# Kernel tuning notes

Hardware: AMD Instinct MI355X
Metric: run time of the kernel (lower is better)

Reference implementation:

```python
import jax, jax.numpy as jnp
import numpy as np

EPS = 1e-6
K = 3
R_MIN, R_MAX = 0.5, 2.0


def setup_inputs() -> dict:
    key = jax.random.key(0)
    k0, k1, k2, k3 = jax.random.split(key, 4)
    N, C, D, H, W = 2, 32, 48, 48, 48
    T = 1 + K + 3 + 1  # num_tokens = 6
    x = jax.random.normal(k0, (N, C, D, H, W), jnp.float32)
    w_field = jax.random.normal(k1, (4 * K, C), jnp.float32) * 0.05
    b_field = jnp.zeros((4 * K,), jnp.float32)
    gates = jax.random.normal(k2, (T,), jnp.float32)
    w_mix = jax.random.normal(k3, (C, T * C), jnp.float32) * 0.02
    b_mix = jnp.zeros((C,), jnp.float32)
    return {"x": x, "w_field": w_field, "b_field": b_field, "gates": gates, "w_mix": w_mix, "b_mix": b_mix}


def _reflect(coord, size):
    # torch 'reflection' padding, align_corners=False: reflect over [-0.5, size-0.5]
    c = jnp.abs(coord + 0.5)
    m = jnp.mod(c, 2.0 * size)
    return jnp.minimum(m, 2.0 * size - m) - 0.5


def _trilinear_sample(vol, gx, gy, gz):
    # vol: (N, D, H, W, C) channels-last; gx/gy/gz: (N, K, D, H, W) normalized coords in [-1, 1]
    N, D, H, W, C = vol.shape

    def unnorm(g, size):
        return _reflect(((g + 1.0) * size - 1.0) * 0.5, float(size))

    ix, iy, iz = unnorm(gx, W), unnorm(gy, H), unnorm(gz, D)
    x0 = jnp.floor(ix); y0 = jnp.floor(iy); z0 = jnp.floor(iz)
    fx = (ix - x0)[..., None]; fy = (iy - y0)[..., None]; fz = (iz - z0)[..., None]
    x0i = jnp.clip(x0.astype(jnp.int32), 0, W - 1); x1i = jnp.clip(x0i + 1, 0, W - 1)
    y0i = jnp.clip(y0.astype(jnp.int32), 0, H - 1); y1i = jnp.clip(y0i + 1, 0, H - 1)
    z0i = jnp.clip(z0.astype(jnp.int32), 0, D - 1); z1i = jnp.clip(z0i + 1, 0, D - 1)
    n = jnp.arange(N).reshape(N, 1, 1, 1, 1)

    def g(zi, yi, xi):
        return vol[n, zi, yi, xi]  # (N, K, D, H, W, C)

    c00 = g(z0i, y0i, x0i) * (1.0 - fx) + g(z0i, y0i, x1i) * fx
    c01 = g(z0i, y1i, x0i) * (1.0 - fx) + g(z0i, y1i, x1i) * fx
    c10 = g(z1i, y0i, x0i) * (1.0 - fx) + g(z1i, y0i, x1i) * fx
    c11 = g(z1i, y1i, x0i) * (1.0 - fx) + g(z1i, y1i, x1i) * fx
    c0 = c00 * (1.0 - fy) + c01 * fy
    c1 = c10 * (1.0 - fy) + c11 * fy
    return c0 * (1.0 - fz) + c1 * fz


def reference(x, w_field, b_field, gates, w_mix, b_mix):
    N, C, D, H, W = x.shape
    # field head: 1x1x1 conv C -> 4K, split into K unit directions U and radii r
    f = jnp.einsum('ncdhw,oc->nodhw', x, w_field) + b_field[None, :, None, None, None]
    f = f.reshape(N, K, 4, D, H, W)
    v = f[:, :, :3]
    U = v / jnp.sqrt(jnp.sum(v * v, axis=2, keepdims=True) + EPS)  # (N,K,3,D,H,W)
    r_s = R_MIN + (R_MAX - R_MIN) * jax.nn.sigmoid(f[:, :, 3])     # (N,K,D,H,W)
    # base grid, align_corners=False normalized coordinates
    gz0 = ((jnp.arange(D, dtype=x.dtype) + 0.5) * 2.0 / D - 1.0)[:, None, None]
    gy0 = ((jnp.arange(H, dtype=x.dtype) + 0.5) * 2.0 / H - 1.0)[None, :, None]
    gx0 = ((jnp.arange(W, dtype=x.dtype) + 0.5) * 2.0 / W - 1.0)[None, None, :]
    ux, uy, uz = U[:, :, 0], U[:, :, 1], U[:, :, 2]
    dx = 2.0 * r_s * ux / (W + EPS)
    dy = 2.0 * r_s * uy / (H + EPS)
    dz = 2.0 * r_s * uz / (D + EPS)
    vol = jnp.transpose(x, (0, 2, 3, 4, 1))  # (N,D,H,W,C)
    xp = _trilinear_sample(vol, gx0 + dx, gy0 + dy, gz0 + dz)  # (N,K,D,H,W,C)
    xm = _trilinear_sample(vol, gx0 - dx, gy0 - dy, gz0 - dz)
    xp = jnp.transpose(xp, (0, 1, 5, 2, 3, 4))  # (N,K,C,D,H,W)
    xm = jnp.transpose(xm, (0, 1, 5, 2, 3, 4))
    a = 0.5 * (xp + xm)
    o = 0.5 * (xp - xm)
    inv_r = 1.0 / (jax.lax.stop_gradient(r_s) + EPS)  # r detached in original
    d1 = o * inv_r[:, :, None]                        # (N,K,C,D,H,W)
    G = jnp.einsum('nkadhw,nkcdhw->nacdhw', U, d1)     # (N,3,C,D,H,W)
    d2 = (xp + xm - 2.0 * x[:, None]) * (inv_r * inv_r)[:, :, None]
    L = d2.mean(axis=1)                                # (N,C,D,H,W)
    tokens = jnp.concatenate([x[:, None], a, G, L[:, None]], axis=1)  # (N,T,C,D,H,W)
    T = tokens.shape[1]
    gated = tokens * jax.nn.sigmoid(gates)[None, :, None, None, None, None]
    delta = jnp.einsum('nmdhw,om->nodhw', gated.reshape(N, T * C, D, H, W), w_mix)
    delta = delta + b_mix[None, :, None, None, None]
    return x + delta
```

## Files before the change

### kernel.cpp

```cpp
#include <hip/hip_runtime.h>
#include <math.h>

#define NB   2
#define CH   32
#define DHW  (48*48*48)
#define TT   8
#define EPSF 1e-6f

#define TILE_N   1521
#define TILE_WSTR 1522
#define GROUPS   8

#define TOK_OFF  0
#define TOK_STR  64
#define TILE_OFF 16384
#define SMEM_SZ  40736

#define WS_BT_F 0
#define WS_WF   4096
#define WS_BF   4480
#define WS_BM   4492

typedef __attribute__((ext_vector_type(8))) short short8;
typedef __attribute__((ext_vector_type(8))) _Float16 half8;
typedef __attribute__((ext_vector_type(4))) float floatx4;
typedef __attribute__((ext_vector_type(2))) _Float16 h2;

struct __align__(8) q4 { h2 lo, hi; };

__device__ __forceinline__ h2 pkrtz(float a, float b) {
    return __builtin_bit_cast(h2, __builtin_amdgcn_cvt_pkrtz(a, b));
}
__device__ __forceinline__ unsigned pkrtz_u(float a, float b) {
    return __builtin_bit_cast(unsigned, __builtin_amdgcn_cvt_pkrtz(a, b));
}

__global__ __launch_bounds__(256) void prep_kernel(
        const float* __restrict__ w_field,
        const float* __restrict__ b_field,
        const float* __restrict__ gates,
        const float* __restrict__ w_mix,
        const float* __restrict__ b_mix,
        float* __restrict__ ws) {
    int i = blockIdx.x * 256 + threadIdx.x;
    {
        int o = i >> 8, k = i & 255, c = k >> 3, t = k & 7;
        float sg = 1.0f / (1.0f + expf(-gates[t]));
        _Float16 hv = (_Float16)(sg * w_mix[o * 256 + t * 32 + c]);
        ((unsigned short*)(ws + WS_BT_F))[o * 256 + k] = __builtin_bit_cast(unsigned short, hv);
    }
    if (i < 384) { int c = i / 12, o = i - c * 12; ws[WS_WF + i] = w_field[o * 32 + c]; }
    if (i < 12)  ws[WS_BF + i] = b_field[i];
    if (i < 32)  ws[WS_BM + i] = b_mix[i];
}

__global__ __launch_bounds__(256) void geo_main(
        const float* __restrict__ x,
        const float* __restrict__ ws,
        float* __restrict__ out) {
    __shared__ __align__(16) char smem[SMEM_SZ];
    char* tokb  = smem + TOK_OFF;
    q4*   tileq = (q4*)(smem + TILE_OFF);
    float* cbuf = (float*)smem;

    const int tid = threadIdx.x;
    const int lin = (blockIdx.x & 7) * 108 + (blockIdx.x >> 3);
    const int bx = lin % 6, by = (lin / 6) % 6, bz = (lin / 36) % 12, n = lin / 432;
    const int lx = tid & 7, ly = (tid >> 3) & 7, lz = tid >> 6;
    const int w = bx * 8 + lx, h = by * 8 + ly, d = bz * 4 + lz;
    const int xlo = bx * 8 - 2, ylo = by * 8 - 2, zlo = bz * 4 - 2;
    const int lane = tid & 63, w64 = tid & 192;

    const float* xn = x + (size_t)n * CH * DHW;

    int goff[6];
#pragma unroll
    for (int i = 0; i < 6; ++i) {
        int e  = tid + i * 256;
        int ee = (e < TILE_N) ? e : 0;
        int tz = ee / 169; int r0 = ee - tz * 169;
        int ty = r0 / 13;  int tx = r0 - ty * 13;
        int zg = min(max(zlo + tz, 0), 47);
        int yg = min(max(ylo + ty, 0), 47);
        int xg = min(max(xlo + tx, 0), 47);
        goff[i] = (zg * 48 + yg) * 48 + xg;
    }

    const int pos = (d * 48 + h) * 48 + w;
    float f[12];
#pragma unroll
    for (int o = 0; o < 12; ++o) f[o] = ws[WS_BF + o];
    for (int c = 0; c < CH; ++c) {
        float xv = xn[c * DHW + pos];
        const float* wf = ws + WS_WF + c * 12;
#pragma unroll
        for (int o = 0; o < 12; ++o) f[o] = fmaf(wf[o], xv, f[o]);
    }

    h2 fx2[6], fy2[6], fz2[6];
    int a00[6], a01[6], a10[6], a11[6];
    float uxk[3], uyk[3], uzk[3], irk[3], ir2k[3];
    const float cscale = 48.0f / (48.0f + EPSF);
#pragma unroll
    for (int k = 0; k < 3; ++k) {
        float vx = f[4*k], vy = f[4*k+1], vz = f[4*k+2], s = f[4*k+3];
        float inv = 1.0f / sqrtf(vx*vx + vy*vy + vz*vz + EPSF);
        float ux = vx * inv, uy = vy * inv, uz = vz * inv;
        float r  = 0.5f + 1.5f / (1.0f + expf(-s));
        uxk[k] = ux; uyk[k] = uy; uzk[k] = uz;
        float ir = 1.0f / (r + EPSF); irk[k] = ir; ir2k[k] = ir * ir;
#pragma unroll
        for (int sgn = 0; sgn < 2; ++sgn) {
            int   si = 2 * k + sgn;
            float sf = sgn ? -1.0f : 1.0f;
            float txr = (float)w + sf * r * ux * cscale;
            float tyr = (float)h + sf * r * uy * cscale;
            float tzr = (float)d + sf * r * uz * cscale;
            float cx = fabsf(txr + 0.5f); float ix = fminf(cx, 96.0f - cx) - 0.5f;
            float cy = fabsf(tyr + 0.5f); float iy = fminf(cy, 96.0f - cy) - 0.5f;
            float cz = fabsf(tzr + 0.5f); float iz = fminf(cz, 96.0f - cz) - 0.5f;
            float x0f = floorf(ix), y0f = floorf(iy), z0f = floorf(iz);
            float fx = ix - x0f, fy = iy - y0f, fz = iz - z0f;
            int x0 = min(max((int)x0f, 0), 47); int x1 = min(x0 + 1, 47);
            int y0 = min(max((int)y0f, 0), 47); int y1 = min(y0 + 1, 47);
            int z0 = min(max((int)z0f, 0), 47); int z1 = min(z0 + 1, 47);
            float fxe = (x1 == x0) ? 0.0f : fx;
            _Float16 hx = (_Float16)fxe, hy = (_Float16)fy, hz = (_Float16)fz;
            fx2[si] = (h2){hx, hx}; fy2[si] = (h2){hy, hy}; fz2[si] = (h2){hz, hz};
            int lz0 = z0 - zlo, lz1 = z1 - zlo;
            int ly0 = y0 - ylo, ly1 = y1 - ylo;
            int lx0 = x0 - xlo;
            a00[si] = (lz0 * 13 + ly0) * 13 + lx0;
            a01[si] = (lz0 * 13 + ly1) * 13 + lx0;
            a10[si] = (lz1 * 13 + ly0) * 13 + lx0;
            a11[si] = (lz1 * 13 + ly1) * 13 + lx0;
        }
    }

    if (tid == 0) {
        q4 z; z.lo = (h2){0, 0}; z.hi = (h2){0, 0};
        tileq[TILE_N] = z; tileq[TILE_WSTR + TILE_N] = z;
    }
    {
        float ld[24];
#pragma unroll
        for (int cg = 0; cg < 4; ++cg) {
            const float* xc = xn + cg * DHW;
#pragma unroll
            for (int i = 0; i < 6; ++i) ld[cg * 6 + i] = xc[goff[i]];
        }
#pragma unroll
        for (int i = 0; i < 6; ++i) {
            int e = tid + i * 256;
            if (e < TILE_N) {
                q4 v; v.lo = pkrtz(ld[i], ld[6 + i]); v.hi = pkrtz(ld[12 + i], ld[18 + i]);
                tileq[e] = v;
            }
        }
    }
    __syncthreads();

    floatx4 acc[4][2];
#pragma unroll
    for (int mt = 0; mt < 4; ++mt)
#pragma unroll
        for (int nt = 0; nt < 2; ++nt) acc[mt][nt] = (floatx4){0.f, 0.f, 0.f, 0.f};

    const int self = ((lz + 2) * 13 + (ly + 2)) * 13 + (lx + 2);
    const unsigned short* bt = (const unsigned short*)(ws + WS_BT_F);
    const int tokq = (tid >> 3) & 3;
    const int qm = lane >> 4, nlo = lane & 15;

    short8 bc0 = *(const short8*)(bt + (nlo * 256 + qm * 8));
    short8 bc1 = *(const short8*)(bt + ((nlo + 16) * 256 + qm * 8));

    for (int g = 0; g < GROUPS; ++g) {
        const int rb = (g & 1);
        const int wb = rb ^ 1;
        float nld[24];
        short8 bn0 = bc0, bn1 = bc1;
        if (g < GROUPS - 1) {
            const float* xg = xn + (g + 1) * 4 * DHW;
#pragma unroll
            for (int cg = 0; cg < 4; ++cg) {
                const float* xc = xg + cg * DHW;
#pragma unroll
                for (int i = 0; i < 6; ++i) nld[cg * 6 + i] = xc[goff[i]];
            }
            bn0 = *(const short8*)(bt + (nlo * 256 + (g + 1) * 32 + qm * 8));
            bn1 = *(const short8*)(bt + ((nlo + 16) * 256 + (g + 1) * 32 + qm * 8));
        }
        const q4* tb = tileq + rb * TILE_WSTR;
        q4 s2 = tb[self];
        q4 vv[6];
#pragma unroll
        for (int si = 0; si < 6; ++si) {
            int b00 = a00[si], b01 = a01[si], b10 = a10[si], b11 = a11[si];
            q4 v000 = tb[b00], v001 = tb[b00 + 1];
            q4 v010 = tb[b01], v011 = tb[b01 + 1];
            q4 v100 = tb[b10], v101 = tb[b10 + 1];
            q4 v110 = tb[b11], v111 = tb[b11 + 1];
            h2 fx = fx2[si], fy = fy2[si], fz = fz2[si];
            h2 c00l = v000.lo + fx * (v001.lo - v000.lo);
            h2 c00h = v000.hi + fx * (v001.hi - v000.hi);
            h2 c01l = v010.lo + fx * (v011.lo - v010.lo);
            h2 c01h = v010.hi + fx * (v011.hi - v010.hi);
            h2 c10l = v100.lo + fx * (v101.lo - v100.lo);
            h2 c10h = v100.hi + fx * (v101.hi - v100.hi);
            h2 c11l = v110.lo + fx * (v111.lo - v110.lo);
            h2 c11h = v110.hi + fx * (v111.hi - v110.hi);
            h2 c0l = c00l + fy * (c01l - c00l);
            h2 c0h = c00h + fy * (c01h - c00h);
            h2 c1l = c10l + fy * (c11l - c10l);
            h2 c1h = c10h + fy * (c11h - c10h);
            vv[si].lo = c0l + fz * (c1l - c0l);
            vv[si].hi = c0h + fz * (c1h - c0h);
        }
#pragma unroll
        for (int sub = 0; sub < 4; ++sub) {
            float xv = (sub == 0) ? (float)s2.lo.x : (sub == 1) ? (float)s2.lo.y
                     : (sub == 2) ? (float)s2.hi.x : (float)s2.hi.y;
            float val[6];
#pragma unroll
            for (int si = 0; si < 6; ++si)
                val[si] = (sub == 0) ? (float)vv[si].lo.x : (sub == 1) ? (float)vv[si].lo.y
                        : (sub == 2) ? (float)vv[si].hi.x : (float)vv[si].hi.y;
            float t1, t2, t3, gx, gy, gz, l;
            {
                float sp, sm, d1;
                sp = val[0]; sm = val[1]; t1 = 0.5f * (sp + sm);
                d1 = 0.5f * (sp - sm) * irk[0];
                gx = uxk[0] * d1; gy = uyk[0] * d1; gz = uzk[0] * d1;
                l  = (sp + sm - 2.0f * xv) * ir2k[0];
                sp = val[2]; sm = val[3]; t2 = 0.5f * (sp + sm);
                d1 = 0.5f * (sp - sm) * irk[1];
                gx = fmaf(uxk[1], d1, gx); gy = fmaf(uyk[1], d1, gy); gz = fmaf(uzk[1], d1, gz);
                l  = fmaf(sp + sm - 2.0f * xv, ir2k[1], l);
                sp = val[4]; sm = val[5]; t3 = 0.5f * (sp + sm);
                d1 = 0.5f * (sp - sm) * irk[2];
                gx = fmaf(uxk[2], d1, gx); gy = fmaf(uyk[2], d1, gy); gz = fmaf(uzk[2], d1, gz);
                l  = fmaf(sp + sm - 2.0f * xv, ir2k[2], l);
            }
            uint4 tw;
            tw.x = pkrtz_u(xv, t1);
            tw.y = pkrtz_u(t2, t3);
            tw.z = pkrtz_u(gx, gy);
            tw.w = pkrtz_u(gz, l * (1.0f / 3.0f));
            int qe = sub ^ tokq;
            *(uint4*)(tokb + tid * TOK_STR + qe * 16) = tw;
        }
        {
            half8 hb0 = __builtin_bit_cast(half8, bc0);
            half8 hb1 = __builtin_bit_cast(half8, bc1);
#pragma unroll
            for (int mt = 0; mt < 4; ++mt) {
                int row = w64 + mt * 16 + nlo;
                int qe  = qm ^ ((row >> 3) & 3);
                half8 a = __builtin_bit_cast(half8,
                          *(const short8*)(tokb + row * TOK_STR + qe * 16));
                acc[mt][0] = __builtin_amdgcn_mfma_f32_16x16x32_f16(a, hb0, acc[mt][0], 0, 0, 0);
                acc[mt][1] = __builtin_amdgcn_mfma_f32_16x16x32_f16(a, hb1, acc[mt][1], 0, 0, 0);
            }
        }
        bc0 = bn0; bc1 = bn1;

        if (g < GROUPS - 1) {
#pragma unroll
            for (int i = 0; i < 6; ++i) {
                int e = tid + i * 256;
                if (e < TILE_N) {
                    q4 v; v.lo = pkrtz(nld[i], nld[6 + i]); v.hi = pkrtz(nld[12 + i], nld[18 + i]);
                    tileq[wb * TILE_WSTR + e] = v;
                }
            }
        }
        __syncthreads();
    }

    {
#pragma unroll
        for (int mt = 0; mt < 4; ++mt)
#pragma unroll
            for (int nt = 0; nt < 2; ++nt)
#pragma unroll
                for (int r = 0; r < 4; ++r) {
                    int v = w64 + mt * 16 + qm * 4 + r;
                    int col = nt * 16 + nlo;
                    cbuf[v * 36 + (col ^ (v & 31))] = acc[mt][nt][r];
                }
    }
    __syncthreads();

    const float* dr = cbuf + tid * 36;
    float* on = out + (size_t)n * CH * DHW;
#pragma unroll
    for (int o = 0; o < 32; ++o)
        __builtin_nontemporal_store(
            xn[o * DHW + pos] + dr[o ^ (tid & 31)] + ws[WS_BM + o],
            on + o * DHW + pos);
}

extern "C" void kernel_launch(void* const* d_in, const int* in_sizes, int n_in,
                              void* d_out, int out_size, void* d_ws, size_t ws_size,
                              hipStream_t stream) {
    const float *x = (const float*)d_in[0], *w_field = (const float*)d_in[1],
                *b_field = (const float*)d_in[2], *gates = (const float*)d_in[3],
                *w_mix = (const float*)d_in[4], *b_mix = (const float*)d_in[5];
    for (int i = 0; i < n_in; ++i) {
        switch (in_sizes[i]) {
            case NB * CH * DHW: x       = (const float*)d_in[i]; break;
            case 12 * CH:       w_field = (const float*)d_in[i]; break;
            case 12:            b_field = (const float*)d_in[i]; break;
            case TT:            gates   = (const float*)d_in[i]; break;
            case CH * TT * CH:  w_mix   = (const float*)d_in[i]; break;
            case CH:            b_mix   = (const float*)d_in[i]; break;
            default: break;
        }
    }
    float* ws = (float*)d_ws;
    prep_kernel<<<32, 256, 0, stream>>>(w_field, b_field, gates, w_mix, b_mix, ws);
    geo_main<<<864, 256, 0, stream>>>(x, ws, (float*)d_out);
}
```

Baseline: 157.0 us.

## Compute token features in packed fp16 and precompute bilinear yz weights

Result: slower. 237.3 us (+51.2%).

```diff
diff --git a/kernel.cpp b/kernel.cpp
--- a/kernel.cpp
+++ b/kernel.cpp
@@ -31,8 +31,11 @@
 __device__ __forceinline__ h2 pkrtz(float a, float b) {
     return __builtin_bit_cast(h2, __builtin_amdgcn_cvt_pkrtz(a, b));
 }
-__device__ __forceinline__ unsigned pkrtz_u(float a, float b) {
-    return __builtin_bit_cast(unsigned, __builtin_amdgcn_cvt_pkrtz(a, b));
+__device__ __forceinline__ h2 dup2(float v) {
+    _Float16 h = (_Float16)v; return (h2){h, h};
+}
+__device__ __forceinline__ unsigned h2u(h2 v) {
+    return __builtin_bit_cast(unsigned, v);
 }
 
 __global__ __launch_bounds__(256) void prep_kernel(
@@ -54,7 +57,7 @@
     if (i < 32)  ws[WS_BM + i] = b_mix[i];
 }
 
-__global__ __launch_bounds__(256) void geo_main(
+__global__ __launch_bounds__(256, 4) void geo_main(
         const float* __restrict__ x,
         const float* __restrict__ ws,
         float* __restrict__ out) {
@@ -97,9 +100,9 @@
         for (int o = 0; o < 12; ++o) f[o] = fmaf(wf[o], xv, f[o]);
     }
 
-    h2 fx2[6], fy2[6], fz2[6];
+    h2 fx2[6], wA[6], wB[6], wC[6], wD[6];
     int a00[6], a01[6], a10[6], a11[6];
-    float uxk[3], uyk[3], uzk[3], irk[3], ir2k[3];
+    h2 hux[3], huy[3], huz[3], hir[3], hq[3];
     const float cscale = 48.0f / (48.0f + EPSF);
 #pragma unroll
     for (int k = 0; k < 3; ++k) {
@@ -107,8 +110,10 @@
         float inv = 1.0f / sqrtf(vx*vx + vy*vy + vz*vz + EPSF);
         float ux = vx * inv, uy = vy * inv, uz = vz * inv;
         float r  = 0.5f + 1.5f / (1.0f + expf(-s));
-        uxk[k] = ux; uyk[k] = uy; uzk[k] = uz;
-        float ir = 1.0f / (r + EPSF); irk[k] = ir; ir2k[k] = ir * ir;
+        float ir = 1.0f / (r + EPSF);
+        hux[k] = dup2(ux); huy[k] = dup2(uy); huz[k] = dup2(uz);
+        hir[k] = dup2(0.5f * ir);
+        hq[k]  = dup2(ir * ir * (1.0f / 3.0f));
 #pragma unroll
         for (int sgn = 0; sgn < 2; ++sgn) {
             int   si = 2 * k + sgn;
@@ -125,8 +130,12 @@
             int y0 = min(max((int)y0f, 0), 47); int y1 = min(y0 + 1, 47);
             int z0 = min(max((int)z0f, 0), 47); int z1 = min(z0 + 1, 47);
             float fxe = (x1 == x0) ? 0.0f : fx;
-            _Float16 hx = (_Float16)fxe, hy = (_Float16)fy, hz = (_Float16)fz;
-            fx2[si] = (h2){hx, hx}; fy2[si] = (h2){hy, hy}; fz2[si] = (h2){hz, hz};
+            fx2[si] = dup2(fxe);
+            float omy = 1.0f - fy, omz = 1.0f - fz;
+            wA[si] = dup2(omy * omz);
+            wB[si] = dup2(fy  * omz);
+            wC[si] = dup2(omy * fz);
+            wD[si] = dup2(fy  * fz);
             int lz0 = z0 - zlo, lz1 = z1 - zlo;
             int ly0 = y0 - ylo, ly1 = y1 - ylo;
             int lx0 = x0 - xlo;
@@ -153,8 +162,8 @@
         for (int i = 0; i < 6; ++i) {
             int e = tid + i * 256;
             if (e < TILE_N) {
-                q4 v; v.lo = pkrtz(ld[i], ld[6 + i]); v.hi = pkrtz(ld[12 + i], ld[18 + i]);
-                tileq[e] = v;
+                q4 vq; vq.lo = pkrtz(ld[i], ld[6 + i]); vq.hi = pkrtz(ld[12 + i], ld[18 + i]);
+                tileq[e] = vq;
             }
         }
     }
@@ -170,6 +179,7 @@
     const unsigned short* bt = (const unsigned short*)(ws + WS_BT_F);
     const int tokq = (tid >> 3) & 3;
     const int qm = lane >> 4, nlo = lane & 15;
+    const h2 HHALF = dup2(0.5f);
 
     short8 bc0 = *(const short8*)(bt + (nlo * 256 + qm * 8));
     short8 bc1 = *(const short8*)(bt + ((nlo + 16) * 256 + qm * 8));
@@ -191,7 +201,7 @@
             bn1 = *(const short8*)(bt + ((nlo + 16) * 256 + (g + 1) * 32 + qm * 8));
         }
         const q4* tb = tileq + rb * TILE_WSTR;
-        q4 s2 = tb[self];
+        q4 sc = tb[self];
         q4 vv[6];
 #pragma unroll
         for (int si = 0; si < 6; ++si) {
@@ -200,54 +210,56 @@
             q4 v010 = tb[b01], v011 = tb[b01 + 1];
             q4 v100 = tb[b10], v101 = tb[b10 + 1];
             q4 v110 = tb[b11], v111 = tb[b11 + 1];
-            h2 fx = fx2[si], fy = fy2[si], fz = fz2[si];
+            h2 fx = fx2[si];
             h2 c00l = v000.lo + fx * (v001.lo - v000.lo);
+            h2 c01l = v010.lo + fx * (v011.lo - v010.lo);
+            h2 c10l = v100.lo + fx * (v101.lo - v100.lo);
+            h2 c11l = v110.lo + fx * (v111.lo - v110.lo);
+            vv[si].lo = (c00l * wA[si] + c01l * wB[si]) + (c10l * wC[si] + c11l * wD[si]);
             h2 c00h = v000.hi + fx * (v001.hi - v000.hi);
-            h2 c01l = v010.lo + fx * (v011.lo - v010.lo);
             h2 c01h = v010.hi + fx * (v011.hi - v010.hi);
-            h2 c10l = v100.lo + fx * (v101.lo - v100.lo);
             h2 c10h = v100.hi + fx * (v101.hi - v100.hi);
-            h2 c11l = v110.lo + fx * (v111.lo - v110.lo);
             h2 c11h = v110.hi + fx * (v111.hi - v110.hi);
-            h2 c0l = c00l + fy * (c01l - c00l);
-            h2 c0h = c00h + fy * (c01h - c00h);
-            h2 c1l = c10l + fy * (c11l - c10l);
-            h2 c1h = c10h + fy * (c11h - c10h);
-            vv[si].lo = c0l + fz * (c1l - c0l);
-            vv[si].hi = c0h + fz * (c1h - c0h);
-        }
-#pragma unroll
-        for (int sub = 0; sub < 4; ++sub) {
-            float xv = (sub == 0) ? (float)s2.lo.x : (sub == 1) ? (float)s2.lo.y
-                     : (sub == 2) ? (float)s2.hi.x : (float)s2.hi.y;
-            float val[6];
-#pragma unroll
-            for (int si = 0; si < 6; ++si)
-                val[si] = (sub == 0) ? (float)vv[si].lo.x : (sub == 1) ? (float)vv[si].lo.y
-                        : (sub == 2) ? (float)vv[si].hi.x : (float)vv[si].hi.y;
-            float t1, t2, t3, gx, gy, gz, l;
-            {
-                float sp, sm, d1;
-                sp = val[0]; sm = val[1]; t1 = 0.5f * (sp + sm);
-                d1 = 0.5f * (sp - sm) * irk[0];
-                gx = uxk[0] * d1; gy = uyk[0] * d1; gz = uzk[0] * d1;
-                l  = (sp + sm - 2.0f * xv) * ir2k[0];
-                sp = val[2]; sm = val[3]; t2 = 0.5f * (sp + sm);
-                d1 = 0.5f * (sp - sm) * irk[1];
-                gx = fmaf(uxk[1], d1, gx); gy = fmaf(uyk[1], d1, gy); gz = fmaf(uzk[1], d1, gz);
-                l  = fmaf(sp + sm - 2.0f * xv, ir2k[1], l);
-                sp = val[4]; sm = val[5]; t3 = 0.5f * (sp + sm);
-                d1 = 0.5f * (sp - sm) * irk[2];
-                gx = fmaf(uxk[2], d1, gx); gy = fmaf(uyk[2], d1, gy); gz = fmaf(uzk[2], d1, gz);
-                l  = fmaf(sp + sm - 2.0f * xv, ir2k[2], l);
-            }
-            uint4 tw;
-            tw.x = pkrtz_u(xv, t1);
-            tw.y = pkrtz_u(t2, t3);
-            tw.z = pkrtz_u(gx, gy);
-            tw.w = pkrtz_u(gz, l * (1.0f / 3.0f));
-            int qe = sub ^ tokq;
-            *(uint4*)(tokb + tid * TOK_STR + qe * 16) = tw;
+            vv[si].hi = (c00h * wA[si] + c01h * wB[si]) + (c10h * wC[si] + c11h * wD[si]);
+        }
+#pragma unroll
+        for (int pr = 0; pr < 2; ++pr) {
+            h2 X  = pr ? sc.hi : sc.lo;
+            h2 V0 = pr ? vv[0].hi : vv[0].lo;
+            h2 V1 = pr ? vv[1].hi : vv[1].lo;
+            h2 V2 = pr ? vv[2].hi : vv[2].lo;
+            h2 V3 = pr ? vv[3].hi : vv[3].lo;
+            h2 V4 = pr ? vv[4].hi : vv[4].lo;
+            h2 V5 = pr ? vv[5].hi : vv[5].lo;
+            h2 xv2 = X + X;
+            h2 s0 = V0 + V1, dm0 = V0 - V1;
+            h2 t1 = HHALF * s0;
+            h2 d0 = dm0 * hir[0];
+            h2 gx = d0 * hux[0], gy = d0 * huy[0], gz = d0 * huz[0];
+            h2 l  = (s0 - xv2) * hq[0];
+            h2 s1 = V2 + V3, dm1 = V2 - V3;
+            h2 t2 = HHALF * s1;
+            h2 d1 = dm1 * hir[1];
+            gx = d1 * hux[1] + gx; gy = d1 * huy[1] + gy; gz = d1 * huz[1] + gz;
+            l  = (s1 - xv2) * hq[1] + l;
+            h2 s2v = V4 + V5, dm2 = V4 - V5;
+            h2 t3 = HHALF * s2v;
+            h2 d2 = dm2 * hir[2];
+            gx = d2 * hux[2] + gx; gy = d2 * huy[2] + gy; gz = d2 * huz[2] + gz;
+            l  = (s2v - xv2) * hq[2] + l;
+            uint4 twa, twb;
+            twa.x = __builtin_amdgcn_perm(h2u(t1), h2u(X),  0x05040100u);
+            twa.y = __builtin_amdgcn_perm(h2u(t3), h2u(t2), 0x05040100u);
+            twa.z = __builtin_amdgcn_perm(h2u(gy), h2u(gx), 0x05040100u);
+            twa.w = __builtin_amdgcn_perm(h2u(l),  h2u(gz), 0x05040100u);
+            twb.x = __builtin_amdgcn_perm(h2u(t1), h2u(X),  0x07060302u);
+            twb.y = __builtin_amdgcn_perm(h2u(t3), h2u(t2), 0x07060302u);
+            twb.z = __builtin_amdgcn_perm(h2u(gy), h2u(gx), 0x07060302u);
+            twb.w = __builtin_amdgcn_perm(h2u(l),  h2u(gz), 0x07060302u);
+            int qa = (2 * pr)     ^ tokq;
+            int qb = (2 * pr + 1) ^ tokq;
+            *(uint4*)(tokb + tid * TOK_STR + qa * 16) = twa;
+            *(uint4*)(tokb + tid * TOK_STR + qb * 16) = twb;
         }
         {
             half8 hb0 = __builtin_bit_cast(half8, bc0);
@@ -269,8 +281,8 @@
             for (int i = 0; i < 6; ++i) {
                 int e = tid + i * 256;
                 if (e < TILE_N) {
-                    q4 v; v.lo = pkrtz(nld[i], nld[6 + i]); v.hi = pkrtz(nld[12 + i], nld[18 + i]);
-                    tileq[wb * TILE_WSTR + e] = v;
+                    q4 vq; vq.lo = pkrtz(nld[i], nld[6 + i]); vq.hi = pkrtz(nld[12 + i], nld[18 + i]);
+                    tileq[wb * TILE_WSTR + e] = vq;
                 }
             }
         }
@@ -284,9 +296,9 @@
             for (int nt = 0; nt < 2; ++nt)
 #pragma unroll
                 for (int r = 0; r < 4; ++r) {
-                    int v = w64 + mt * 16 + qm * 4 + r;
+                    int vr = w64 + mt * 16 + qm * 4 + r;
                     int col = nt * 16 + nlo;
-                    cbuf[v * 36 + (col ^ (v & 31))] = acc[mt][nt][r];
+                    cbuf[vr * 36 + (col ^ (vr & 31))] = acc[mt][nt][r];
                 }
     }
     __syncthreads();
```
